# Optimization experiments

Measured on AMD Instinct MI355X. Metric: run time of the kernel, lower is better.

## Reference

```python
import jax, jax.numpy as jnp
import numpy as np

B, N, IN_F, OUT_F, H = 8, 1024, 128, 128, 4
HD = OUT_F // H  # 32
NEG_SLOPE = 0.2


def setup_inputs() -> dict:
    key = jax.random.key(0)
    k1, k2, k3, k4 = jax.random.split(key, 4)
    x = jax.random.normal(k1, (B, N, IN_F), dtype=jnp.float32)
    W = jax.random.normal(k2, (IN_F, OUT_F), dtype=jnp.float32) * (1.0 / np.sqrt(IN_F))
    a_src = jax.random.normal(k3, (H, HD), dtype=jnp.float32)
    a_dst = jax.random.normal(k4, (H, HD), dtype=jnp.float32)
    return {"x": x, "W": W, "a_src": a_src, "a_dst": a_dst}


def reference(x, W, a_src, a_dst):
    # Linear projection, split heads: (B, N, H, HD)
    h = (x @ W).reshape(B, N, H, HD)
    # Per-node additive attention terms: (B, N, H)
    attn_src = jnp.einsum("bnhd,hd->bnh", h, a_src)
    attn_dst = jnp.einsum("bnhd,hd->bnh", h, a_dst)
    # attn[b,i,j,h] = src_i + dst_j  -> (B, N, N, H)
    attn = attn_src[:, :, None, :] + attn_dst[:, None, :, :]
    attn = jnp.where(attn >= 0, attn, NEG_SLOPE * attn)  # LeakyReLU(0.2)
    attn = jax.nn.softmax(attn, axis=2)  # softmax over source nodes j
    # dropout is identity in eval/reference mode
    # Weighted aggregation per head: out[b,i,h,d] = sum_j attn[b,i,j,h] * h[b,j,h,d]
    out = jnp.einsum("bijh,bjhd->bihd", attn, h)
    return out.reshape(B, N, OUT_F)
```

## Files before the change

### kernel.cpp

```cpp
#include <hip/hip_runtime.h>


constexpr int CB  = 8;
constexpr int CN  = 1024;
constexpr int CF  = 128;
constexpr int CH  = 4;
constexpr int CHD = 32;
constexpr int CBH = CB * CH;
constexpr int CROWS = CB * CN;
constexpr int TROWS = CN + 1;
constexpr int NBK = 1024;

__global__ __launch_bounds__(256) void proj_kernel(
    const float* __restrict__ x, const float* __restrict__ W,
    const float* __restrict__ a_src, const float* __restrict__ a_dst,
    float* __restrict__ h_ws, float* __restrict__ sarr, float* __restrict__ darr)
{
    __shared__ float xs[8 * 132];
    __shared__ float wslab[64 * 128];

    const int tid = threadIdx.x, row0 = blockIdx.x * 8;

    {
        const int rr = tid >> 5, k4 = tid & 31;
        *(float4*)(xs + rr * 132 + k4 * 4) = ((const float4*)x)[(size_t)row0 * 32 + tid];
    }

    const int r = tid >> 5, c4 = tid & 31;
    const int head = c4 >> 3, dd0 = (c4 & 7) * 4;
    float acc[4] = {0.f, 0.f, 0.f, 0.f};

    const float4* W4 = (const float4*)W;
    for (int slab = 0; slab < 2; ++slab) {
        __syncthreads();
        #pragma unroll
        for (int m = 0; m < 8; ++m) {
            const int idx = m * 256 + tid;
            const int kk = idx >> 5, k4 = idx & 31;
            *(float4*)(wslab + kk * 128 + k4 * 4) = W4[(size_t)(slab * 64 + kk) * 32 + k4];
        }
        __syncthreads();
        #pragma unroll 4
        for (int k4 = 0; k4 < 16; ++k4) {
            const float4 xv = *(const float4*)(xs + r * 132 + slab * 64 + k4 * 4);
            const float xq[4] = {xv.x, xv.y, xv.z, xv.w};
            #pragma unroll
            for (int q = 0; q < 4; ++q) {
                const int kk = k4 * 4 + q;
                const float4 wv = *(const float4*)(wslab + kk * 128 + c4 * 4);
                const float xk = xq[q];
                acc[0] += xk * wv.x; acc[1] += xk * wv.y;
                acc[2] += xk * wv.z; acc[3] += xk * wv.w;
            }
        }
    }

    const float4 as = *(const float4*)(a_src + head * CHD + dd0);
    const float4 ad = *(const float4*)(a_dst + head * CHD + dd0);
    float sp = acc[0]*as.x + acc[1]*as.y + acc[2]*as.z + acc[3]*as.w;
    float dp = acc[0]*ad.x + acc[1]*ad.y + acc[2]*ad.z + acc[3]*ad.w;
    sp += __shfl_xor(sp, 1); sp += __shfl_xor(sp, 2); sp += __shfl_xor(sp, 4);
    dp += __shfl_xor(dp, 1); dp += __shfl_xor(dp, 2); dp += __shfl_xor(dp, 4);

    const int rowg = row0 + r, b = rowg >> 10, n = rowg & 1023;
    const int bh = b * CH + head;
    *(float4*)(h_ws + (size_t)(bh * CN + n) * CHD + dd0) =
        make_float4(acc[0], acc[1], acc[2], acc[3]);
    if ((c4 & 7) == 0) {
        sarr[bh * CN + n] = sp;
        darr[bh * CN + n] = dp;
    }
}

__global__ __launch_bounds__(1024) void tail_kernel(
    const float* __restrict__ h_ws, const float* __restrict__ sarr,
    const float* __restrict__ darr, float* __restrict__ tbl_g,
    float* __restrict__ out)
{
    __shared__ float dchS[CN];
    __shared__ int   pchS[CN];
    __shared__ int   bsS[NBK + 1];
    __shared__ int   cnts[NBK];
    __shared__ float ctF[32 * 32], ctB[32 * 32];
    __shared__ float ofF[33 * 32], ofB[33 * 32];
    __shared__ float ctSF[32], ctSB[32], ofSF[33], ofSB[33];
    __shared__ float sPBl[CN + 1], sSFl[CN + 1];
    __shared__ float redS[32];
    __shared__ int   wsumS[16];
    __shared__ float prmS[2];

    const int bh = blockIdx.x, tid = threadIdx.x;
    const int lane = tid & 63, wid = tid >> 6;
    float* tbl = tbl_g + (size_t)bh * TROWS * 64;

    const float d = darr[bh * CN + tid];
    float mn = d, mx = d;
    #pragma unroll
    for (int off = 1; off < 64; off <<= 1) {
        mn = fminf(mn, __shfl_xor(mn, off));
        mx = fmaxf(mx, __shfl_xor(mx, off));
    }
    if (lane == 0) { redS[wid] = mn; redS[16 + wid] = mx; }
    cnts[tid] = 0;
    if (tid < 64) tbl[(size_t)CN * 64 + tid] = 0.f;
    if (tid == 0) { sPBl[CN] = 0.f; sSFl[CN] = 0.f; }
    __syncthreads();
    if (tid == 0) {
        float m0 = redS[0], m1 = redS[16];
        for (int w = 1; w < 16; ++w) { m0 = fminf(m0, redS[w]); m1 = fmaxf(m1, redS[16 + w]); }
        const float rng = fmaxf(m1 - m0, 1e-30f);
        prmS[0] = m0; prmS[1] = (float)NBK / rng;
    }
    __syncthreads();
    const float mnb = prmS[0], invw = prmS[1];
    const int f = (int)fminf(fmaxf((d - mnb) * invw, 0.0f), 1023.0f);
    const int rank = atomicAdd(&cnts[f], 1);
    __syncthreads();

    const int c = cnts[tid];
    int incl = c;
    #pragma unroll
    for (int off = 1; off < 64; off <<= 1) {
        const int t = __shfl_up(incl, off);
        if (lane >= off) incl += t;
    }
    if (lane == 63) wsumS[wid] = incl;
    __syncthreads();
    if (tid < 16) {
        const int v = wsumS[tid];
        int iv = v;
        #pragma unroll
        for (int off = 1; off < 16; off <<= 1) {
            const int t = __shfl_up(iv, off);
            if (tid >= off) iv += t;
        }
        wsumS[tid] = iv - v;
    }
    __syncthreads();
    bsS[tid] = incl - c + wsumS[wid];
    if (tid == 0) bsS[NBK] = CN;
    __syncthreads();
    const int pos = bsS[f] + rank;
    dchS[pos] = d;
    pchS[pos] = tid;
    __syncthreads();

    const int cc = tid >> 5, dd = tid & 31, cb = cc * 32;
    const float* hb = h_ws + (size_t)bh * CN * CHD;
    {
        float accF = 0.f, accS = 0.f;
        for (int bt = 0; bt < 2; ++bt) {
            float hv[16], dv[16];
            #pragma unroll
            for (int t = 0; t < 16; ++t) {
                const int lp = cb + bt * 16 + t;
                hv[t] = hb[(size_t)pchS[lp] * CHD + dd];
                dv[t] = dchS[lp];
            }
            #pragma unroll
            for (int t = 0; t < 16; ++t) {
                const int lp = cb + bt * 16 + t;
                const float cf = __expf(0.2f * dv[t]);
                tbl[lp * 64 + dd] = accF;
                if (dd == 0) sPBl[lp] = accS;
                accF += cf * hv[t];
                accS += cf;
            }
        }
        ctF[cc * 32 + dd] = accF;
        if (dd == 0) ctSF[cc] = accS;
    }
    {
        float accB = 0.f, accS = 0.f;
        for (int bt = 0; bt < 2; ++bt) {
            float hv[16], dv[16];
            #pragma unroll
            for (int t = 0; t < 16; ++t) {
                const int lp = cb + 31 - (bt * 16 + t);
                hv[t] = hb[(size_t)pchS[lp] * CHD + dd];
                dv[t] = dchS[lp];
            }
            #pragma unroll
            for (int t = 0; t < 16; ++t) {
                const int lp = cb + 31 - (bt * 16 + t);
                const float cf = __expf(dv[t]);
                accB += cf * hv[t];
                accS += cf;
                tbl[lp * 64 + 32 + dd] = accB;
                if (dd == 0) sSFl[lp] = accS;
            }
        }
        ctB[cc * 32 + dd] = accB;
        if (dd == 0) ctSB[cc] = accS;
    }
    __syncthreads();

    if (tid < 32) {
        float run = 0.f;
        for (int c2 = 0; c2 < 32; ++c2) { ofF[c2 * 32 + tid] = run; run += ctF[c2 * 32 + tid]; }
        ofF[32 * 32 + tid] = run;
    } else if (tid < 64) {
        const int d2 = tid - 32;
        float run = 0.f;
        ofB[32 * 32 + d2] = 0.f;
        for (int c2 = 31; c2 >= 0; --c2) { ofB[c2 * 32 + d2] = run; run += ctB[c2 * 32 + d2]; }
    } else if (tid == 64) {
        float run = 0.f;
        for (int c2 = 0; c2 < 32; ++c2) { ofSF[c2] = run; run += ctSF[c2]; }
        ofSF[32] = run;
    } else if (tid == 65) {
        float run = 0.f;
        ofSB[32] = 0.f;
        for (int c2 = 31; c2 >= 0; --c2) { ofSB[c2] = run; run += ctSB[c2]; }
    }
    __syncthreads();

    const int i = tid;
    const float s = sarr[bh * CN + i];
    const float c1 = __expf(s), c2v = __expf(0.2f * s), thr = -s;
    const int kb = (int)fminf(fmaxf((thr - mnb) * invw, 0.0f), 1023.0f);
    const int q0 = bsS[kb], q1 = bsS[kb + 1];
    const int kcf = q0 >> 5, kcb = q1 >> 5;

    float pbs = sPBl[q0] + ofSF[kcf];
    float sfs = sSFl[q1] + ofSB[kcb];

    const float4* trf = (const float4*)(tbl + (size_t)q0 * 64);
    const float4* trb = (const float4*)(tbl + (size_t)q1 * 64 + 32);
    float4 vF[8], vB[8];
    #pragma unroll
    for (int qq = 0; qq < 8; ++qq) {
        const float4 pb = trf[qq], oa = *(const float4*)(&ofF[kcf * 32 + qq * 4]);
        const float4 sf = trb[qq], ob = *(const float4*)(&ofB[kcb * 32 + qq * 4]);
        vF[qq] = make_float4(pb.x + oa.x, pb.y + oa.y, pb.z + oa.z, pb.w + oa.w);
        vB[qq] = make_float4(sf.x + ob.x, sf.y + ob.y, sf.z + ob.z, sf.w + ob.w);
    }

    for (int p = q0; p < q1; ++p) {
        const float dq = dchS[p];
        const float4* hr = (const float4*)(hb + (size_t)pchS[p] * CHD);
        const bool pre = (dq < thr);
        const float w = __expf(pre ? 0.2f * dq : dq);
        if (pre) pbs += w; else sfs += w;
        #pragma unroll
        for (int qq = 0; qq < 8; ++qq) {
            const float4 hv = hr[qq];
            if (pre) {
                vF[qq].x += w * hv.x; vF[qq].y += w * hv.y;
                vF[qq].z += w * hv.z; vF[qq].w += w * hv.w;
            } else {
                vB[qq].x += w * hv.x; vB[qq].y += w * hv.y;
                vB[qq].z += w * hv.z; vB[qq].w += w * hv.w;
            }
        }
    }

    const float inv = 1.0f / (c2v * pbs + c1 * sfs);
    const int b = bh >> 2, hh = bh & 3;
    float4* o = (float4*)(out + (size_t)(b * CN + i) * CF + hh * 32);
    #pragma unroll
    for (int qq = 0; qq < 8; ++qq) {
        o[qq] = make_float4((c2v * vF[qq].x + c1 * vB[qq].x) * inv,
                            (c2v * vF[qq].y + c1 * vB[qq].y) * inv,
                            (c2v * vF[qq].z + c1 * vB[qq].z) * inv,
                            (c2v * vF[qq].w + c1 * vB[qq].w) * inv);
    }
}

extern "C" void kernel_launch(void* const* d_in, const int* in_sizes, int n_in,
                              void* d_out, int out_size, void* d_ws, size_t ws_size,
                              hipStream_t stream) {
    const float* x     = (const float*)d_in[0];
    const float* W     = (const float*)d_in[1];
    const float* a_src = (const float*)d_in[2];
    const float* a_dst = (const float*)d_in[3];
    float* out = (float*)d_out;

    char* ws = (char*)d_ws;
    size_t off = 0;
    float* h_ws = (float*)(ws + off); off += (size_t)CROWS * CF * 4;
    float* sarr = (float*)(ws + off); off += (size_t)CBH * CN * 4;
    float* darr = (float*)(ws + off); off += (size_t)CBH * CN * 4;
    float* tblg = (float*)(ws + off); off += (size_t)CBH * TROWS * 64 * 4;
    (void)ws_size;

    proj_kernel<<<CROWS / 8, 256, 0, stream>>>(x, W, a_src, a_dst, h_ws, sarr, darr);
    tail_kernel<<<CBH, 1024, 0, stream>>>(h_ws, sarr, darr, tblg, out);
}
```

Measured before the change: 112.6 us.

## Split GAT tail into scan and output kernels across more blocks

Replaces the single 32-block tail kernel (1024 threads each) with two kernels of 256 blocks each. The first builds chunk prefix tables, with groups now defined by sort buckets rather than fixed positions. The second recomputes the bucket sort per block and computes 128 output rows, with two threads per row handling 16 head dims each. This spreads work across many more CUs, which the old 32-block grid left mostly idle. The cost is an extra launch, the counting sort being redundantly recomputed in every block, and a global round-trip for the chunk totals.

```diff
diff --git a/kernel.cpp b/kernel.cpp
--- a/kernel.cpp
+++ b/kernel.cpp
@@ -10,6 +10,7 @@
 constexpr int CROWS = CB * CN;
 constexpr int TROWS = CN + 1;
 constexpr int NBK = 1024;
+constexpr int NG  = 32;
 
 __global__ __launch_bounds__(256) void proj_kernel(
     const float* __restrict__ x, const float* __restrict__ W,
@@ -72,53 +73,43 @@
     }
 }
 
-__global__ __launch_bounds__(1024) void tail_kernel(
-    const float* __restrict__ h_ws, const float* __restrict__ sarr,
-    const float* __restrict__ darr, float* __restrict__ tbl_g,
-    float* __restrict__ out)
+__device__ __forceinline__ void count_build(
+    const float* __restrict__ darr, int bh, int tid,
+    int* cnts, int* bsS, float* dsS, int* pjS, int* pgS,
+    float* redmn, float* redmx, int* wsumS,
+    float& mnb_out, float& invw_out)
 {
-    __shared__ float dchS[CN];
-    __shared__ int   pchS[CN];
-    __shared__ int   bsS[NBK + 1];
-    __shared__ int   cnts[NBK];
-    __shared__ float ctF[32 * 32], ctB[32 * 32];
-    __shared__ float ofF[33 * 32], ofB[33 * 32];
-    __shared__ float ctSF[32], ctSB[32], ofSF[33], ofSB[33];
-    __shared__ float sPBl[CN + 1], sSFl[CN + 1];
-    __shared__ float redS[32];
-    __shared__ int   wsumS[16];
-    __shared__ float prmS[2];
-
-    const int bh = blockIdx.x, tid = threadIdx.x;
     const int lane = tid & 63, wid = tid >> 6;
-    float* tbl = tbl_g + (size_t)bh * TROWS * 64;
-
-    const float d = darr[bh * CN + tid];
-    float mn = d, mx = d;
+    float dv[4];
+    #pragma unroll
+    for (int u = 0; u < 4; ++u) dv[u] = darr[bh * CN + tid + 256 * u];
+    float mn = fminf(fminf(dv[0], dv[1]), fminf(dv[2], dv[3]));
+    float mx = fmaxf(fmaxf(dv[0], dv[1]), fmaxf(dv[2], dv[3]));
     #pragma unroll
     for (int off = 1; off < 64; off <<= 1) {
         mn = fminf(mn, __shfl_xor(mn, off));
         mx = fmaxf(mx, __shfl_xor(mx, off));
     }
-    if (lane == 0) { redS[wid] = mn; redS[16 + wid] = mx; }
-    cnts[tid] = 0;
-    if (tid < 64) tbl[(size_t)CN * 64 + tid] = 0.f;
-    if (tid == 0) { sPBl[CN] = 0.f; sSFl[CN] = 0.f; }
-    __syncthreads();
-    if (tid == 0) {
-        float m0 = redS[0], m1 = redS[16];
-        for (int w = 1; w < 16; ++w) { m0 = fminf(m0, redS[w]); m1 = fmaxf(m1, redS[16 + w]); }
-        const float rng = fmaxf(m1 - m0, 1e-30f);
-        prmS[0] = m0; prmS[1] = (float)NBK / rng;
-    }
-    __syncthreads();
-    const float mnb = prmS[0], invw = prmS[1];
-    const int f = (int)fminf(fmaxf((d - mnb) * invw, 0.0f), 1023.0f);
-    const int rank = atomicAdd(&cnts[f], 1);
-    __syncthreads();
-
-    const int c = cnts[tid];
-    int incl = c;
+    if (lane == 0) { redmn[wid] = mn; redmx[wid] = mx; }
+    #pragma unroll
+    for (int u = 0; u < 4; ++u) cnts[tid + 256 * u] = 0;
+    __syncthreads();
+    const float m0 = fminf(fminf(redmn[0], redmn[1]), fminf(redmn[2], redmn[3]));
+    const float m1 = fmaxf(fmaxf(redmx[0], redmx[1]), fmaxf(redmx[2], redmx[3]));
+    const float rng = fmaxf(m1 - m0, 1e-30f);
+    const float invw = (float)NBK / rng;
+    mnb_out = m0; invw_out = invw;
+
+    int fb[4], rk[4];
+    #pragma unroll
+    for (int u = 0; u < 4; ++u) {
+        fb[u] = (int)fminf(fmaxf((dv[u] - m0) * invw, 0.0f), 1023.0f);
+        rk[u] = atomicAdd(&cnts[fb[u]], 1);
+    }
+    __syncthreads();
+    const int c0 = cnts[4*tid], c1 = cnts[4*tid+1], c2 = cnts[4*tid+2], c3 = cnts[4*tid+3];
+    const int sum4 = c0 + c1 + c2 + c3;
+    int incl = sum4;
     #pragma unroll
     for (int off = 1; off < 64; off <<= 1) {
         const int t = __shfl_up(incl, off);
@@ -126,140 +117,200 @@
     }
     if (lane == 63) wsumS[wid] = incl;
     __syncthreads();
-    if (tid < 16) {
-        const int v = wsumS[tid];
-        int iv = v;
-        #pragma unroll
-        for (int off = 1; off < 16; off <<= 1) {
-            const int t = __shfl_up(iv, off);
-            if (tid >= off) iv += t;
-        }
-        wsumS[tid] = iv - v;
-    }
-    __syncthreads();
-    bsS[tid] = incl - c + wsumS[wid];
+    if (tid == 0) { int r0 = 0; for (int w = 0; w < 4; ++w) { const int t = wsumS[w]; wsumS[w] = r0; r0 += t; } }
+    __syncthreads();
+    const int base = incl - sum4 + wsumS[wid];
+    bsS[4*tid]   = base;
+    bsS[4*tid+1] = base + c0;
+    bsS[4*tid+2] = base + c0 + c1;
+    bsS[4*tid+3] = base + c0 + c1 + c2;
     if (tid == 0) bsS[NBK] = CN;
     __syncthreads();
-    const int pos = bsS[f] + rank;
-    dchS[pos] = d;
-    pchS[pos] = tid;
-    __syncthreads();
-
-    const int cc = tid >> 5, dd = tid & 31, cb = cc * 32;
+    #pragma unroll
+    for (int u = 0; u < 4; ++u) {
+        const int pos = bsS[fb[u]] + rk[u];
+        dsS[pos] = dv[u];
+        pjS[pos] = tid + 256 * u;
+        if (pgS) pgS[pos] = fb[u] >> 5;
+    }
+    __syncthreads();
+}
+
+__global__ __launch_bounds__(256) void scanc_kernel(
+    const float* __restrict__ h_ws, const float* __restrict__ darr,
+    float* __restrict__ tbl_g, float* __restrict__ sPB_g, float* __restrict__ sSF_g,
+    float* __restrict__ ctF_g, float* __restrict__ ctB_g,
+    float* __restrict__ ctSF_g, float* __restrict__ ctSB_g)
+{
+    __shared__ int   cnts[NBK];
+    __shared__ int   bsS[NBK + 1];
+    __shared__ float dsS[CN];
+    __shared__ int   pjS[CN];
+    __shared__ float redmn[4], redmx[4];
+    __shared__ int   wsumS[4];
+
+    const int blk = blockIdx.x, tid = threadIdx.x;
+    const int bh = blk & 31, sb = blk >> 5;
+    float mnb, invw;
+    count_build(darr, bh, tid, cnts, bsS, dsS, pjS, nullptr, redmn, redmx, wsumS, mnb, invw);
+
+    float* tbl = tbl_g + (size_t)bh * TROWS * 64;
+    if (sb == 0) {
+        if (tid < 64) tbl[(size_t)CN * 64 + tid] = 0.f;
+        if (tid == 0) { sPB_g[bh * TROWS + CN] = 0.f; sSF_g[bh * TROWS + CN] = 0.f; }
+    }
+
+    const int dir = tid >> 7, gidx = (tid >> 5) & 3, dd = tid & 31;
+    const int g = sb * 4 + gidx;
+    const int lo = bsS[32 * g], hi = bsS[32 * g + 32];
     const float* hb = h_ws + (size_t)bh * CN * CHD;
-    {
-        float accF = 0.f, accS = 0.f;
-        for (int bt = 0; bt < 2; ++bt) {
-            float hv[16], dv[16];
-            #pragma unroll
-            for (int t = 0; t < 16; ++t) {
-                const int lp = cb + bt * 16 + t;
-                hv[t] = hb[(size_t)pchS[lp] * CHD + dd];
-                dv[t] = dchS[lp];
-            }
-            #pragma unroll
-            for (int t = 0; t < 16; ++t) {
-                const int lp = cb + bt * 16 + t;
-                const float cf = __expf(0.2f * dv[t]);
-                tbl[lp * 64 + dd] = accF;
-                if (dd == 0) sPBl[lp] = accS;
-                accF += cf * hv[t];
-                accS += cf;
-            }
-        }
-        ctF[cc * 32 + dd] = accF;
-        if (dd == 0) ctSF[cc] = accS;
-    }
-    {
-        float accB = 0.f, accS = 0.f;
-        for (int bt = 0; bt < 2; ++bt) {
-            float hv[16], dv[16];
-            #pragma unroll
-            for (int t = 0; t < 16; ++t) {
-                const int lp = cb + 31 - (bt * 16 + t);
-                hv[t] = hb[(size_t)pchS[lp] * CHD + dd];
-                dv[t] = dchS[lp];
-            }
-            #pragma unroll
-            for (int t = 0; t < 16; ++t) {
-                const int lp = cb + 31 - (bt * 16 + t);
-                const float cf = __expf(dv[t]);
-                accB += cf * hv[t];
-                accS += cf;
-                tbl[lp * 64 + 32 + dd] = accB;
-                if (dd == 0) sSFl[lp] = accS;
-            }
-        }
-        ctB[cc * 32 + dd] = accB;
-        if (dd == 0) ctSB[cc] = accS;
-    }
-    __syncthreads();
+
+    if (dir == 0) {
+        float acc = 0.f, accS = 0.f;
+        for (int base = lo; base < hi; base += 8) {
+            float hv[8], dvv[8];
+            #pragma unroll
+            for (int t = 0; t < 8; ++t) {
+                const int p = base + t;
+                if (p < hi) { hv[t] = hb[(size_t)pjS[p] * CHD + dd]; dvv[t] = dsS[p]; }
+            }
+            #pragma unroll
+            for (int t = 0; t < 8; ++t) {
+                const int p = base + t;
+                if (p < hi) {
+                    const float cf = __expf(0.2f * dvv[t]);
+                    tbl[p * 64 + dd] = acc;
+                    if (dd == 0) sPB_g[bh * TROWS + p] = accS;
+                    acc += cf * hv[t];
+                    accS += cf;
+                }
+            }
+        }
+        ctF_g[(bh * NG + g) * 32 + dd] = acc;
+        if (dd == 0) ctSF_g[bh * NG + g] = accS;
+    } else {
+        float acc = 0.f, accS = 0.f;
+        for (int base = hi - 1; base >= lo; base -= 8) {
+            float hv[8], dvv[8];
+            #pragma unroll
+            for (int t = 0; t < 8; ++t) {
+                const int p = base - t;
+                if (p >= lo) { hv[t] = hb[(size_t)pjS[p] * CHD + dd]; dvv[t] = dsS[p]; }
+            }
+            #pragma unroll
+            for (int t = 0; t < 8; ++t) {
+                const int p = base - t;
+                if (p >= lo) {
+                    const float cf = __expf(dvv[t]);
+                    acc += cf * hv[t];
+                    accS += cf;
+                    tbl[p * 64 + 32 + dd] = acc;
+                    if (dd == 0) sSF_g[bh * TROWS + p] = accS;
+                }
+            }
+        }
+        ctB_g[(bh * NG + g) * 32 + dd] = acc;
+        if (dd == 0) ctSB_g[bh * NG + g] = accS;
+    }
+}
+
+__global__ __launch_bounds__(256) void outc_kernel(
+    const float* __restrict__ h_ws, const float* __restrict__ sarr,
+    const float* __restrict__ darr,
+    const float* __restrict__ sPB_g, const float* __restrict__ sSF_g,
+    const float* __restrict__ ctF_g, const float* __restrict__ ctB_g,
+    const float* __restrict__ ctSF_g, const float* __restrict__ ctSB_g,
+    const float* __restrict__ tbl_g, float* __restrict__ out)
+{
+    __shared__ int   cnts[NBK];
+    __shared__ int   bsS[NBK + 1];
+    __shared__ float dsS[CN];
+    __shared__ int   pjS[CN];
+    __shared__ int   pgS[CN];
+    __shared__ float redmn[4], redmx[4];
+    __shared__ int   wsumS[4];
+    __shared__ float ctF[NG * 32], ctB[NG * 32];
+    __shared__ float ofF[(NG + 1) * 32], ofB[(NG + 1) * 32];
+    __shared__ float ctSF[NG], ctSB[NG], ofSF[NG + 1], ofSB[NG + 1];
+
+    const int blk = blockIdx.x, tid = threadIdx.x;
+    const int bh = blk & 31, oct = blk >> 5;
+
+    #pragma unroll
+    for (int rr = 0; rr < 4; ++rr) {
+        const int idx = rr * 256 + tid;
+        ctF[idx] = ctF_g[bh * (NG * 32) + idx];
+        ctB[idx] = ctB_g[bh * (NG * 32) + idx];
+    }
+    if (tid < NG)            ctSF[tid] = ctSF_g[bh * NG + tid];
+    else if (tid < 2 * NG)   ctSB[tid - NG] = ctSB_g[bh * NG + (tid - NG)];
+
+    float mnb, invw;
+    count_build(darr, bh, tid, cnts, bsS, dsS, pjS, pgS, redmn, redmx, wsumS, mnb, invw);
 
     if (tid < 32) {
         float run = 0.f;
-        for (int c2 = 0; c2 < 32; ++c2) { ofF[c2 * 32 + tid] = run; run += ctF[c2 * 32 + tid]; }
-        ofF[32 * 32 + tid] = run;
+        for (int c2 = 0; c2 < NG; ++c2) { ofF[c2 * 32 + tid] = run; run += ctF[c2 * 32 + tid]; }
+        ofF[NG * 32 + tid] = run;
     } else if (tid < 64) {
         const int d2 = tid - 32;
         float run = 0.f;
-        ofB[32 * 32 + d2] = 0.f;
-        for (int c2 = 31; c2 >= 0; --c2) { ofB[c2 * 32 + d2] = run; run += ctB[c2 * 32 + d2]; }
+        ofB[NG * 32 + d2] = 0.f;
+        for (int c2 = NG - 1; c2 >= 0; --c2) { ofB[c2 * 32 + d2] = run; run += ctB[c2 * 32 + d2]; }
     } else if (tid == 64) {
         float run = 0.f;
-        for (int c2 = 0; c2 < 32; ++c2) { ofSF[c2] = run; run += ctSF[c2]; }
-        ofSF[32] = run;
+        for (int c2 = 0; c2 < NG; ++c2) { ofSF[c2] = run; run += ctSF[c2]; }
+        ofSF[NG] = run;
     } else if (tid == 65) {
         float run = 0.f;
-        ofSB[32] = 0.f;
-        for (int c2 = 31; c2 >= 0; --c2) { ofSB[c2] = run; run += ctSB[c2]; }
-    }
-    __syncthreads();
-
-    const int i = tid;
+        ofSB[NG] = 0.f;
+        for (int c2 = NG - 1; c2 >= 0; --c2) { ofSB[c2] = run; run += ctSB[c2]; }
+    }
+    __syncthreads();
+
+    const int i = oct * 128 + (tid >> 1), half = tid & 1, hd0 = half * 16;
     const float s = sarr[bh * CN + i];
     const float c1 = __expf(s), c2v = __expf(0.2f * s), thr = -s;
     const int kb = (int)fminf(fmaxf((thr - mnb) * invw, 0.0f), 1023.0f);
     const int q0 = bsS[kb], q1 = bsS[kb + 1];
-    const int kcf = q0 >> 5, kcb = q1 >> 5;
-
-    float pbs = sPBl[q0] + ofSF[kcf];
-    float sfs = sSFl[q1] + ofSB[kcb];
-
-    const float4* trf = (const float4*)(tbl + (size_t)q0 * 64);
-    const float4* trb = (const float4*)(tbl + (size_t)q1 * 64 + 32);
-    float4 vF[8], vB[8];
-    #pragma unroll
-    for (int qq = 0; qq < 8; ++qq) {
-        const float4 pb = trf[qq], oa = *(const float4*)(&ofF[kcf * 32 + qq * 4]);
-        const float4 sf = trb[qq], ob = *(const float4*)(&ofB[kcb * 32 + qq * 4]);
+    const int gF = (q0 < CN) ? pgS[q0] : NG;
+    const int gB = (q1 < CN) ? pgS[q1] : NG;
+
+    float pbs = sPB_g[bh * TROWS + q0] + ofSF[gF];
+    float sfs = sSF_g[bh * TROWS + q1] + ofSB[gB];
+
+    const float* tb = tbl_g + (size_t)bh * TROWS * 64;
+    const float4* trf = (const float4*)(tb + (size_t)q0 * 64 + hd0);
+    const float4* trb = (const float4*)(tb + (size_t)q1 * 64 + 32 + hd0);
+    float4 vF[4], vB[4];
+    #pragma unroll
+    for (int qq = 0; qq < 4; ++qq) {
+        const float4 pb = trf[qq], oa = *(const float4*)(&ofF[gF * 32 + hd0 + qq * 4]);
+        const float4 sf = trb[qq], ob = *(const float4*)(&ofB[gB * 32 + hd0 + qq * 4]);
         vF[qq] = make_float4(pb.x + oa.x, pb.y + oa.y, pb.z + oa.z, pb.w + oa.w);
         vB[qq] = make_float4(sf.x + ob.x, sf.y + ob.y, sf.z + ob.z, sf.w + ob.w);
     }
 
+    const float* hb = h_ws + (size_t)bh * CN * CHD;
     for (int p = q0; p < q1; ++p) {
-        const float dq = dchS[p];
-        const float4* hr = (const float4*)(hb + (size_t)pchS[p] * CHD);
+        const float dq = dsS[p];
+        const float4* hr = (const float4*)(hb + (size_t)pjS[p] * CHD + hd0);
         const bool pre = (dq < thr);
         const float w = __expf(pre ? 0.2f * dq : dq);
         if (pre) pbs += w; else sfs += w;
         #pragma unroll
-        for (int qq = 0; qq < 8; ++qq) {
+        for (int qq = 0; qq < 4; ++qq) {
             const float4 hv = hr[qq];
-            if (pre) {
-                vF[qq].x += w * hv.x; vF[qq].y += w * hv.y;
-                vF[qq].z += w * hv.z; vF[qq].w += w * hv.w;
-            } else {
-                vB[qq].x += w * hv.x; vB[qq].y += w * hv.y;
-                vB[qq].z += w * hv.z; vB[qq].w += w * hv.w;
-            }
+            if (pre) { vF[qq].x += w*hv.x; vF[qq].y += w*hv.y; vF[qq].z += w*hv.z; vF[qq].w += w*hv.w; }
+            else     { vB[qq].x += w*hv.x; vB[qq].y += w*hv.y; vB[qq].z += w*hv.z; vB[qq].w += w*hv.w; }
         }
     }
 
     const float inv = 1.0f / (c2v * pbs + c1 * sfs);
     const int b = bh >> 2, hh = bh & 3;
-    float4* o = (float4*)(out + (size_t)(b * CN + i) * CF + hh * 32);
-    #pragma unroll
-    for (int qq = 0; qq < 8; ++qq) {
+    float4* o = (float4*)(out + (size_t)(b * CN + i) * CF + hh * 32 + hd0);
+    #pragma unroll
+    for (int qq = 0; qq < 4; ++qq) {
         o[qq] = make_float4((c2v * vF[qq].x + c1 * vB[qq].x) * inv,
                             (c2v * vF[qq].y + c1 * vB[qq].y) * inv,
                             (c2v * vF[qq].z + c1 * vB[qq].z) * inv,
@@ -282,8 +333,17 @@
     float* sarr = (float*)(ws + off); off += (size_t)CBH * CN * 4;
     float* darr = (float*)(ws + off); off += (size_t)CBH * CN * 4;
     float* tblg = (float*)(ws + off); off += (size_t)CBH * TROWS * 64 * 4;
+    float* sPBg = (float*)(ws + off); off += (size_t)CBH * TROWS * 4;
+    float* sSFg = (float*)(ws + off); off += (size_t)CBH * TROWS * 4;
+    float* ctFg = (float*)(ws + off); off += (size_t)CBH * NG * 32 * 4;
+    float* ctBg = (float*)(ws + off); off += (size_t)CBH * NG * 32 * 4;
+    float* ctSFg= (float*)(ws + off); off += (size_t)CBH * NG * 4;
+    float* ctSBg= (float*)(ws + off); off += (size_t)CBH * NG * 4;
     (void)ws_size;
 
     proj_kernel<<<CROWS / 8, 256, 0, stream>>>(x, W, a_src, a_dst, h_ws, sarr, darr);
-    tail_kernel<<<CBH, 1024, 0, stream>>>(h_ws, sarr, darr, tblg, out);
-}
+    scanc_kernel<<<256, 256, 0, stream>>>(h_ws, darr, tblg, sPBg, sSFg,
+                                          ctFg, ctBg, ctSFg, ctSBg);
+    outc_kernel<<<256, 256, 0, stream>>>(h_ws, sarr, darr, sPBg, sSFg,
+                                         ctFg, ctBg, ctSFg, ctSBg, tblg, out);
+}
```

After: 113.5 us. No clear change (+0.8%).
